# Performance work log

Measured on AMD Instinct MI355X. Metric: run time of the kernel, lower is better.

The kernel has to match this reference:

```python
import jax, jax.numpy as jnp
import numpy as np

L0, L1, L2 = 32, 16, 8
NS, NB = 512, 256
CUT = 7.0
N, E, G = 16384, 131072, 16
FEAT = L0 + 3 * L1 + 5 * L2  # 120


def setup_inputs() -> dict:
    key = jax.random.key(0)
    ks = jax.random.split(key, 16)
    rn = lambda k, s, sc=1.0: jax.random.normal(k, s, jnp.float32) * sc
    inp = {}
    inp['nodes'] = rn(ks[0], (N, FEAT))
    inp['pos'] = rn(ks[1], (N, 3)) * 5.0
    inp['cell'] = rn(ks[2], (G, 3, 3))
    inp['edge_shift'] = rn(ks[3], (E, 3))
    # tensor-product path weights (e3nn FullyConnectedTensorProduct, uvw mode)
    inp['W0'] = rn(ks[4], (L0, L0, NS))
    inp['W1'] = rn(ks[5], (L1, L1, NS))
    inp['W2'] = rn(ks[6], (L2, L2, NS))
    inp['ln_g'] = jnp.ones((NS,), jnp.float32)
    inp['ln_b'] = jnp.zeros((NS,), jnp.float32)
    inp['df_w1'] = rn(ks[7], (NB, 1024), NB ** -0.5)
    inp['df_b1'] = jnp.zeros((1024,), jnp.float32)
    inp['df_w2'] = rn(ks[8], (1024, NS), 1024 ** -0.5)
    inp['df_b2'] = jnp.zeros((NS,), jnp.float32)
    inp['mi_w1'] = rn(ks[9], (NS, 1024), NS ** -0.5)
    inp['mi_b1'] = jnp.zeros((1024,), jnp.float32)
    inp['mi_w2'] = rn(ks[10], (1024, 1024), 1024 ** -0.5)
    inp['mi_b2'] = jnp.zeros((1024,), jnp.float32)
    inp['mo_w'] = rn(ks[11], (1024, 1), 1024 ** -0.5)
    inp['mo_b'] = jnp.zeros((1,), jnp.float32)
    inp['edge_index'] = jax.random.randint(ks[12], (2, E), 0, N)
    inp['batch_vec'] = jnp.sort(jax.random.randint(ks[13], (N,), 0, G))
    return inp


def _split_irreps(x):
    x0 = x[:, :L0]                                   # (E, L0) scalars 0e
    x1 = x[:, L0:L0 + 3 * L1].reshape(-1, L1, 3)      # (E, L1, 3) vectors 1o
    x2 = x[:, L0 + 3 * L1:].reshape(-1, L2, 5)        # (E, L2, 5) 2e
    return x0, x1, x2


def reference(nodes, pos, cell, edge_shift, W0, W1, W2, ln_g, ln_b,
              df_w1, df_b1, df_w2, df_b2, mi_w1, mi_b1, mi_w2, mi_b2,
              mo_w, mo_b, edge_index, batch_vec):
    src, dst = edge_index[0], edge_index[1]
    # periodic-image translation vector per edge
    bcell = cell[batch_vec[src]]                      # (E,3,3)
    tvec = jnp.einsum('ei,eij->ej', edge_shift, bcell)
    radvec = pos[dst] - pos[src] + tvec               # (E,3)
    dist = jnp.linalg.norm(radvec, axis=1, keepdims=True)  # (E,1)
    r = 1.0 / (dist + 1e-6)
    # Bessel radial embedding with cutoff CUT, NB basis functions
    n = jnp.arange(1, NB + 1, dtype=jnp.float32)
    emb = jnp.sqrt(2.0 / CUT) * jnp.sin(n * jnp.pi * r / CUT) / r  # (E,NB)
    distfilter = jax.nn.silu(emb @ df_w1 + df_b1) @ df_w2 + df_b2  # (E,NS)

    # symmetrized fully-connected tensor product -> 0e scalars
    # 0.5*(tp(xs,xd)+tp(xd,xs)) == contraction of euv with symmetrized W
    xs0, xs1, xs2 = _split_irreps(nodes[src])
    xd0, xd1, xd2 = _split_irreps(nodes[dst])
    fan = jnp.sqrt(jnp.float32(L0 * L0 + L1 * L1 + L2 * L2))  # element path norm
    sym = lambda W: 0.5 * (W + W.transpose(1, 0, 2))
    e0 = jnp.einsum('eu,ev->euv', xs0, xd0)
    mixed = jnp.einsum('euv,uvw->ew', e0, sym(W0)) / fan
    e1 = jnp.einsum('eui,evi->euv', xs1, xd1)
    mixed = mixed + jnp.einsum('euv,uvw->ew', e1, sym(W1)) / (fan * jnp.sqrt(3.0))
    e2 = jnp.einsum('eui,evi->euv', xs2, xd2)
    mixed = mixed + jnp.einsum('euv,uvw->ew', e2, sym(W2)) / (fan * jnp.sqrt(5.0))

    # LayerNorm over numscalars
    mu = jnp.mean(mixed, axis=-1, keepdims=True)
    var = jnp.mean((mixed - mu) ** 2, axis=-1, keepdims=True)
    mixednorm = (mixed - mu) * jax.lax.rsqrt(var + 1e-5) * ln_g + ln_b

    reg = mixednorm * distfilter
    h = jax.nn.silu(reg @ mi_w1 + mi_b1)
    h = jax.nn.silu(h @ mi_w2 + mi_b2)
    return h @ mo_w + mo_b  # (E,1)
```

## Files before the change

kernel.cpp:

```cpp
#include <hip/hip_runtime.h>

#define EE 131072
#define NNODE 16384
#define FEAT 120
#define NS 512
#define NB 256
#define KCAT 1344

typedef unsigned short u16;
typedef __bf16 bf16x8 __attribute__((ext_vector_type(8)));
typedef float f32x4 __attribute__((ext_vector_type(4)));
typedef unsigned short ushort8 __attribute__((ext_vector_type(8)));
typedef unsigned short us4 __attribute__((ext_vector_type(4)));

__device__ __forceinline__ float b2f(u16 u) {
  union { unsigned int i; float f; } x; x.i = ((unsigned int)u) << 16; return x.f;
}
__device__ __forceinline__ u16 f2b(float f) {
  union { float f; unsigned int i; } x; x.f = f;
  unsigned int lsb = (x.i >> 16) & 1u;
  x.i += 0x7fffu + lsb;
  return (u16)(x.i >> 16);
}
__device__ __forceinline__ u16 f2b_fast(float f) {
  __bf16 h = (__bf16)f;
  union { __bf16 h; u16 u; } x; x.h = h; return x.u;
}
__device__ __forceinline__ float rdany(const void* p, long i, int f32) {
  return f32 ? ((const float*)p)[i] : b2f(((const u16*)p)[i]);
}

__device__ __forceinline__ void gload16(const u16* g, u16* l) {
  __builtin_amdgcn_global_load_lds(
      (__attribute__((address_space(1))) void*)(u16*)g,
      (__attribute__((address_space(3))) void*)l, 16, 0, 0);
}

struct PrepArgs {
  long cum[20];
  const void* src[19];
  u16* dst[19];
  float* outf;
  int* flag;
  const u16* nodes;
};

__global__ __launch_bounds__(256) void megaprep(PrepArgs a) {
  __shared__ int scnt[4];
  {
    u16 v = a.nodes[threadIdx.x];
    int e = (v >> 7) & 0xFF;
    unsigned long long b = __ballot(e >= 0x48);
    if ((threadIdx.x & 63) == 0) scnt[threadIdx.x >> 6] = __popcll(b);
  }
  __syncthreads();
  const int f32 = (scnt[0] + scnt[1] + scnt[2] + scnt[3]) >= 16;
  if (blockIdx.x == 0 && threadIdx.x == 0) *a.flag = f32;

  long i = (long)blockIdx.x * 256 + threadIdx.x;
  const long total = a.cum[19];
  if (i < total) {
    int s = 0;
    while (i >= a.cum[s + 1]) s++;
    long local = i - a.cum[s];
    a.dst[s][local] = f32 ? f2b(((const float*)a.src[s])[local])
                          : ((const u16*)a.src[s])[local];
  } else {
    long j = i - total;
    if (j < EE) a.outf[j] = 0.f;
  }
}

struct WprepArgs {
  const u16* tin[4];
  u16* tout[4];
  const u16 *W0, *W1, *W2;
  u16* wcT;
};

__device__ __forceinline__ void do_transpose(const u16* in, u16* out, int R, int C, int rem) {
  __shared__ u16 tile[32][33];
  const int bx = C >> 5;
  const int c0 = (rem % bx) * 32, r0 = (rem / bx) * 32;
  const int tx = threadIdx.x & 31, ty = threadIdx.x >> 5;
  for (int i = 0; i < 32; i += 8) {
    int r = r0 + ty + i, c = c0 + tx;
    if (r < R && c < C) tile[ty + i][tx] = in[(long)r * C + c];
  }
  __syncthreads();
  for (int i = 0; i < 32; i += 8) {
    int r = r0 + tx, c = c0 + ty + i;
    if (r < R && c < C) out[(long)c * R + r] = tile[tx][ty + i];
  }
}

__global__ __launch_bounds__(256) void wprep(WprepArgs a) {
  int b = blockIdx.x;
  if (b < 256) { do_transpose(a.tin[0], a.tout[0], 256, 1024, b); return; }
  b -= 256;
  if (b < 512) { do_transpose(a.tin[1], a.tout[1], 1024, 512, b); return; }
  b -= 512;
  if (b < 512) { do_transpose(a.tin[2], a.tout[2], 512, 1024, b); return; }
  b -= 512;
  if (b < 1024) { do_transpose(a.tin[3], a.tout[3], 1024, 1024, b); return; }
  b -= 1024;
  int idx = b * 256 + threadIdx.x;
  if (idx >= NS * KCAT) return;
  int w = idx / KCAT, k = idx - w * KCAT;
  const float fan = 36.66060556f;
  float val;
  if (k < 1024) {
    int u = k >> 5, v = k & 31;
    val = 0.5f * (b2f(a.W0[(u * 32 + v) * NS + w]) + b2f(a.W0[(v * 32 + u) * NS + w])) / fan;
  } else if (k < 1280) {
    int j = k - 1024;
    int u = j >> 4, v = j & 15;
    val = 0.5f * (b2f(a.W1[(u * 16 + v) * NS + w]) + b2f(a.W1[(v * 16 + u) * NS + w])) /
          (fan * 1.7320508076f);
  } else {
    int j = k - 1280;
    int u = j >> 3, v = j & 7;
    val = 0.5f * (b2f(a.W2[(u * 8 + v) * NS + w]) + b2f(a.W2[(v * 8 + u) * NS + w])) /
          (fan * 2.2360679775f);
  }
  a.wcT[idx] = f2b(val);
}

__global__ __launch_bounds__(256) void edge_prep(
    const u16* __restrict__ nodes, const void* __restrict__ pos, const void* __restrict__ cell,
    const void* __restrict__ shift, const int* __restrict__ eidx, const int* __restrict__ batch,
    u16* __restrict__ emb, u16* __restrict__ ocat, int e0, const int* __restrict__ flag) {
  const int wave = threadIdx.x >> 6, lane = threadIdx.x & 63;
  const int el = blockIdx.x * 4 + wave;
  const int e = e0 + el;
  const int f32 = *flag;
  __shared__ u16 sxs[4][FEAT], sxd[4][FEAT];
  const int src = eidx[e], dst = eidx[EE + e];
  for (int i = lane; i < FEAT; i += 64) {
    sxs[wave][i] = nodes[(long)src * FEAT + i];
    sxd[wave][i] = nodes[(long)dst * FEAT + i];
  }
  __syncthreads();
  const int b = batch[src];
  float s0 = rdany(shift, (long)e * 3, f32), s1 = rdany(shift, (long)e * 3 + 1, f32),
        s2 = rdany(shift, (long)e * 3 + 2, f32);
  float d2 = 0.f;
#pragma unroll
  for (int j = 0; j < 3; j++) {
    float tv = s0 * rdany(cell, b * 9 + j, f32) + s1 * rdany(cell, b * 9 + 3 + j, f32) +
               s2 * rdany(cell, b * 9 + 6 + j, f32);
    float rv = rdany(pos, dst * 3 + j, f32) - rdany(pos, src * 3 + j, f32) + tv;
    d2 += rv * rv;
  }
  float dist = sqrtf(d2);
  float r = 1.0f / (dist + 1e-6f);
  const float c0 = 0.5345224838f;
  const float pi7 = 0.44879895051f;
  {
    us4 ev;
#pragma unroll
    for (int j = 0; j < 4; j++) {
      int n = lane * 4 + j;
      ev[j] = f2b(c0 * sinf((float)(n + 1) * pi7 * r) / r);
    }
    *(us4*)&emb[(long)el * NB + lane * 4] = ev;
  }
  const u16* xs = sxs[wave];
  const u16* xd = sxd[wave];
  u16* orow = ocat + (long)el * KCAT;
  {
    const float xu = b2f(xs[lane >> 1]);
    const int v0 = (lane & 1) * 16;
    const ushort8 xd0 = *(const ushort8*)&xd[v0];
    const ushort8 xd1 = *(const ushort8*)&xd[v0 + 8];
    ushort8 o0, o1;
#pragma unroll
    for (int j = 0; j < 8; j++) {
      o0[j] = f2b(xu * b2f(xd0[j]));
      o1[j] = f2b(xu * b2f(xd1[j]));
    }
    *(ushort8*)&orow[lane * 16] = o0;
    *(ushort8*)&orow[lane * 16 + 8] = o1;
  }
  {
    const int u = lane >> 2;
    us4 o;
#pragma unroll
    for (int j = 0; j < 4; j++) {
      const int v = (lane & 3) * 4 + j;
      float s = 0.f;
#pragma unroll
      for (int i = 0; i < 3; i++) s += b2f(xs[32 + u * 3 + i]) * b2f(xd[32 + v * 3 + i]);
      o[j] = f2b(s);
    }
    *(us4*)&orow[1024 + lane * 4] = o;
  }
  {
    int u = lane >> 3, v = lane & 7;
    float s = 0.f;
#pragma unroll
    for (int i = 0; i < 5; i++) s += b2f(xs[80 + u * 5 + i]) * b2f(xd[80 + v * 5 + i]);
    orow[1280 + lane] = f2b(s);
  }
}

#define STGA(buf, h, part, kk)                                             \
  gload16(Ag + ((h)*128 + (part)*64) * (long)K + (kk),                      \
          &lA[buf][(h)*8192 + (part)*4096 + tid * 8])
#define STGB(buf, h, part, kk)                                             \
  gload16(Bg + ((h)*128 + (part)*64) * (long)K + (kk),                      \
          &lB[buf][(h)*8192 + (part)*4096 + tid * 8])
#define RDA(buf, fm, ks)                                                   \
  (*(const bf16x8*)((const char*)&lA[buf][0] +                             \
                    ((wm * 128 + (fm)*16 + row_l) * 128 + ((ks) ? ir1 : ir0))))
#define RDB(buf, fn, ks)                                                   \
  (*(const bf16x8*)((const char*)&lB[buf][0] +                             \
                    ((wn * 64 + (fn)*16 + row_l) * 128 + ((ks) ? ir1 : ir0))))
#define MF16(a, b, c) __builtin_amdgcn_mfma_f32_16x16x32_bf16(a, b, c, 0, 0, 0)
#define MFQn(mh, nh, Af, Bf)                                               \
  do {                                                                     \
    _Pragma("unroll") for (int f = 0; f < 4; f++)                          \
        _Pragma("unroll") for (int g = 0; g < 2; g++)                      \
            _Pragma("unroll") for (int ks = 0; ks < 2; ks++)               \
                acc[(mh)*4 + f][(nh)*2 + g] =                              \
        MF16(Af[f][ks], Bf[g][ks], acc[(mh)*4 + f][(nh)*2 + g]);           \
  } while (0)

template <int ACT, int OF32, int HEAD>
__global__ __launch_bounds__(512, 2) void gemm_bt(const u16* __restrict__ A,
                                                  const u16* __restrict__ BT,
                                                  const u16* __restrict__ bias,
                                                  void* __restrict__ Cv,
                                                  const u16* __restrict__ hw,
                                                  float* __restrict__ outf, int N, int K) {
  __shared__ __align__(16) u16 lA[2][16384];
  __shared__ __align__(16) u16 lB[2][16384];
  const int tid = threadIdx.x;
  const int lane = tid & 63;
  const int wave = tid >> 6;
  const int wm = wave >> 2, wn = wave & 3;
  const int row_l = lane & 15;
  const int kq16 = (lane >> 4) << 4;
  const int swz = (row_l & 7) << 4;
  const int ir0 = kq16 ^ swz;
  const int ir1 = (64 + kq16) ^ swz;

  const int nbn = N >> 8;
  int idx = blockIdx.x;
  if ((gridDim.x & 7) == 0) {
    int per = gridDim.x >> 3;
    idx = (blockIdx.x & 7) * per + (blockIdx.x >> 3);
  }
  const int mi = idx / nbn;
  const int ni = idx - mi * nbn;
  const long m0 = (long)mi * 256;
  const int n0 = ni << 8;
  const int nk = K >> 6;

  const int srow = tid >> 3;
  const int gseg = (tid & 7) ^ (srow & 7);
  const u16* Ag = A + (m0 + srow) * (long)K + gseg * 8;
  const u16* Bg = BT + (long)(n0 + srow) * K + gseg * 8;

  f32x4 acc[8][4];
#pragma unroll
  for (int i = 0; i < 8; i++)
#pragma unroll
    for (int j = 0; j < 4; j++)
#pragma unroll
      for (int q = 0; q < 4; q++) acc[i][j][q] = 0.f;

  STGA(0, 0, 0, 0); STGA(0, 0, 1, 0); STGA(0, 1, 0, 0); STGA(0, 1, 1, 0);
  STGB(0, 0, 0, 0); STGB(0, 0, 1, 0); STGB(0, 1, 0, 0); STGB(0, 1, 1, 0);
  if (nk > 1) {
    STGA(1, 0, 0, 64); STGA(1, 0, 1, 64); STGA(1, 1, 0, 64); STGA(1, 1, 1, 64);
    STGB(1, 0, 0, 64); STGB(1, 0, 1, 64); STGB(1, 1, 0, 64); STGB(1, 1, 1, 64);
    asm volatile("s_waitcnt vmcnt(8)" ::: "memory");
  } else {
    asm volatile("s_waitcnt vmcnt(0)" ::: "memory");
  }
  __builtin_amdgcn_s_barrier();

  bf16x8 af0[4][2], af1[4][2], b01[2][2], b23[2][2];

#pragma unroll
  for (int f = 0; f < 4; f++) { af0[f][0] = RDA(0, f, 0); af0[f][1] = RDA(0, f, 1); }
#pragma unroll
  for (int g = 0; g < 2; g++) { b01[g][0] = RDB(0, g, 0); b01[g][1] = RDB(0, g, 1); }

  for (int t = 0; t < nk; ++t) {
    const int cur = t & 1, nxt = cur ^ 1;
    const int kN2 = (t + 2) << 6;
    const bool p1 = (t + 1) < nk;
    const bool p2 = (t + 2) < nk;

#pragma unroll
    for (int g = 0; g < 2; g++) { b23[g][0] = RDB(cur, 2 + g, 0); b23[g][1] = RDB(cur, 2 + g, 1); }
    __builtin_amdgcn_sched_barrier(0);
    __builtin_amdgcn_s_setprio(1);
    MFQn(0, 0, af0, b01);
    __builtin_amdgcn_s_setprio(0);

#pragma unroll
    for (int f = 0; f < 4; f++) { af1[f][0] = RDA(cur, 4 + f, 0); af1[f][1] = RDA(cur, 4 + f, 1); }
    __builtin_amdgcn_sched_barrier(0);
    __builtin_amdgcn_s_setprio(1);
    MFQn(0, 1, af0, b23);
    __builtin_amdgcn_s_setprio(0);

    asm volatile("s_waitcnt vmcnt(0)" ::: "memory");
    __builtin_amdgcn_s_barrier();
    if (p1) {
#pragma unroll
      for (int f = 0; f < 4; f++) { af0[f][0] = RDA(nxt, f, 0); af0[f][1] = RDA(nxt, f, 1); }
    }
    if (p2) { STGB(cur, 0, 0, kN2); STGB(cur, 0, 1, kN2); }
    __builtin_amdgcn_sched_barrier(0);
    __builtin_amdgcn_s_setprio(1);
    MFQn(1, 0, af1, b01);
    __builtin_amdgcn_s_setprio(0);

    __builtin_amdgcn_s_barrier();
    if (p2) {
      STGB(cur, 1, 0, kN2); STGB(cur, 1, 1, kN2);
      STGA(cur, 0, 0, kN2); STGA(cur, 0, 1, kN2);
      STGA(cur, 1, 0, kN2); STGA(cur, 1, 1, kN2);
    }
    __builtin_amdgcn_sched_barrier(0);
    __builtin_amdgcn_s_setprio(1);
    MFQn(1, 1, af1, b23);
    __builtin_amdgcn_s_setprio(0);
    if (p1) {
#pragma unroll
      for (int g = 0; g < 2; g++) { b01[g][0] = RDB(nxt, g, 0); b01[g][1] = RDB(nxt, g, 1); }
      __builtin_amdgcn_sched_barrier(0);
    }
  }

  const int rql = (lane >> 4) * 2;
  const int cl = lane & 15;
  float* Cf = (float*)Cv;
  u16* Cb = (u16*)Cv;
  if (HEAD) {
    float bv[4], hv[4];
#pragma unroll
    for (int g = 0; g < 4; g++) {
      const int col = n0 + wn * 64 + g * 16 + cl;
      bv[g] = b2f(bias[col]);
      hv[g] = b2f(hw[col]);
    }
#pragma unroll
    for (int fm = 0; fm < 8; fm++) {
#pragma unroll
      for (int q = 0; q < 4; q++) {
        float s = 0.f;
#pragma unroll
        for (int g = 0; g < 4; g++) {
          float v = acc[fm][g][q] + bv[g];
          if (ACT) v = __fdividef(v, 1.0f + __expf(-v));
          s += v * hv[g];
        }
        s += __shfl_xor(s, 1);
        s += __shfl_xor(s, 2);
        s += __shfl_xor(s, 4);
        s += __shfl_xor(s, 8);
        if (cl == 0) {
          long row = m0 + wm * 128 + fm * 16 + rql * 2 + q;
          atomicAdd(&outf[row], s);
        }
      }
    }
  } else {
#pragma unroll
    for (int fm = 0; fm < 8; fm++) {
#pragma unroll
      for (int g = 0; g < 4; g++) {
        const int col = n0 + wn * 64 + g * 16 + cl;
        const float bvv = bias ? b2f(bias[col]) : 0.0f;
#pragma unroll
        for (int q = 0; q < 4; q++) {
          long row = m0 + wm * 128 + fm * 16 + rql * 2 + q;
          float v = acc[fm][g][q] + bvv;
          if (ACT) v = __fdividef(v, 1.0f + __expf(-v));
          if (OF32)
            Cf[row * N + col] = v;
          else
            Cb[row * N + col] = f2b_fast(v);
        }
      }
    }
  }
}

__global__ __launch_bounds__(256) void ln_mul_k(const float* __restrict__ mixed,
                                                const u16* __restrict__ g,
                                                const u16* __restrict__ bvec,
                                                u16* __restrict__ dfreg) {
  const int wave = threadIdx.x >> 6, lane = threadIdx.x & 63;
  const long e = (long)blockIdx.x * 4 + wave;
  const float* row = mixed + e * NS;
  float x[8];
  f32x4 v0 = *(const f32x4*)&row[lane * 8];
  f32x4 v1 = *(const f32x4*)&row[lane * 8 + 4];
#pragma unroll
  for (int j = 0; j < 4; j++) { x[j] = v0[j]; x[4 + j] = v1[j]; }
  float s = 0.f, sq = 0.f;
#pragma unroll
  for (int j = 0; j < 8; j++) { s += x[j]; sq += x[j] * x[j]; }
  for (int o = 32; o; o >>= 1) { s += __shfl_xor(s, o); sq += __shfl_xor(sq, o); }
  float mu = s * (1.0f / 512.0f);
  float var = sq * (1.0f / 512.0f) - mu * mu;
  float rstd = rsqrtf(var + 1e-5f);
  u16* drow = dfreg + e * NS;
  ushort8 dv = *(const ushort8*)&drow[lane * 8];
  ushort8 ov;
#pragma unroll
  for (int j = 0; j < 8; j++) {
    int c = lane * 8 + j;
    float val = (x[j] - mu) * rstd * b2f(g[c]) + b2f(bvec[c]);
    ov[j] = f2b(val * b2f(dv[j]));
  }
  *(ushort8*)&drow[lane * 8] = ov;
}

__global__ __launch_bounds__(256) void head_finish(const float* __restrict__ outf,
                                                   const u16* __restrict__ b,
                                                   void* __restrict__ out,
                                                   const int* __restrict__ flag) {
  int e = blockIdx.x * 256 + threadIdx.x;
  float v = outf[e] + b2f(b[0]);
  if (*flag)
    ((float*)out)[e] = v;
  else
    ((u16*)out)[e] = f2b(v);
}

extern "C" void kernel_launch(void* const* d_in, const int* in_sizes, int n_in, void* d_out,
                              int out_size, void* d_ws, size_t ws_size, hipStream_t stream) {
  const int* eidx = (const int*)d_in[19];
  const int* batch = (const int*)d_in[20];

  char* ws = (char*)d_ws;
  size_t off = 0;
  auto alloc = [&](size_t bytes) {
    char* p = ws + off;
    off += (bytes + 255) & ~(size_t)255;
    return p;
  };

  int* flag = (int*)alloc(256);
  float* outf = (float*)alloc((size_t)EE * 4);

  PrepArgs pa;
  u16* cv[19];
  long cum = 0;
  for (int i = 0; i < 19; i++) {
    long n = in_sizes[i];
    cv[i] = (u16*)alloc((size_t)n * 2);
    pa.cum[i] = cum;
    pa.src[i] = d_in[i];
    pa.dst[i] = cv[i];
    cum += n;
  }
  pa.cum[19] = cum;
  pa.outf = outf;
  pa.flag = flag;
  pa.nodes = (const u16*)d_in[0];
  {
    long tot = cum + EE;
    megaprep<<<(int)((tot + 255) / 256), 256, 0, stream>>>(pa);
  }
  const u16* nodes = cv[0];
  const u16* ln_g = cv[7];
  const u16* ln_b = cv[8];
  const u16* df_b1 = cv[10];
  const u16* df_b2 = cv[12];
  const u16* mi_b1 = cv[14];
  const u16* mi_b2 = cv[16];
  const u16* mo_w = cv[17];
  const u16* mo_b = cv[18];

  u16* w1T = (u16*)alloc(1024 * 256 * 2);
  u16* w2T = (u16*)alloc(512 * 1024 * 2);
  u16* m1T = (u16*)alloc(1024 * 512 * 2);
  u16* m2T = (u16*)alloc((size_t)1024 * 1024 * 2);
  u16* wcT = (u16*)alloc((size_t)NS * KCAT * 2);

  WprepArgs wa;
  wa.tin[0] = cv[9];  wa.tout[0] = w1T;
  wa.tin[1] = cv[11]; wa.tout[1] = w2T;
  wa.tin[2] = cv[13]; wa.tout[2] = m1T;
  wa.tin[3] = cv[15]; wa.tout[3] = m2T;
  wa.W0 = cv[4]; wa.W1 = cv[5]; wa.W2 = cv[6];
  wa.wcT = wcT;
  wprep<<<4992, 256, 0, stream>>>(wa);

  int nchunk = 1;
  while (nchunk < 64) {
    size_t CHs = (size_t)(EE / nchunk);
    size_t need = off + CHs * 6272 + 8192;
    if (need <= ws_size) break;
    nchunk <<= 1;
  }
  const int CH = EE / nchunk;

  u16* ocat = (u16*)alloc((size_t)CH * KCAT * 2);
  u16* emb = (u16*)alloc((size_t)CH * NB * 2);
  u16* h1 = (u16*)alloc((size_t)CH * 1024 * 2);
  u16* dfb = (u16*)alloc((size_t)CH * NS * 2);
  u16* h2 = ocat;
  float* mixed = (float*)h1;

  const int RB = CH / 256;
  for (int c = 0; c < nchunk; c++) {
    const int eb = c * CH;
    edge_prep<<<CH / 4, 256, 0, stream>>>(nodes, d_in[1], d_in[2], d_in[3], eidx, batch, emb,
                                          ocat, eb, flag);

    gemm_bt<1, 0, 0><<<RB * 4, 512, 0, stream>>>(emb, w1T, df_b1, h1, nullptr, nullptr, 1024, 256);
    gemm_bt<0, 0, 0><<<RB * 2, 512, 0, stream>>>(h1, w2T, df_b2, dfb, nullptr, nullptr, 512, 1024);

    gemm_bt<0, 1, 0><<<RB * 2, 512, 0, stream>>>(ocat, wcT, nullptr, mixed, nullptr, nullptr, 512,
                                                 1344);

    ln_mul_k<<<CH / 4, 256, 0, stream>>>(mixed, ln_g, ln_b, dfb);

    gemm_bt<1, 0, 0><<<RB * 4, 512, 0, stream>>>(dfb, m1T, mi_b1, h2, nullptr, nullptr, 1024, 512);
    gemm_bt<1, 0, 1><<<RB * 4, 512, 0, stream>>>(h2, m2T, mi_b2, nullptr, mo_w, outf + eb, 1024,
                                                 1024);
  }
  head_finish<<<EE / 256, 256, 0, stream>>>(outf, mo_b, d_out, flag);
}
```

Measured before the change: 1.335 ms.

## Fuse independent distfilter-1 and tensor-product GEMMs into one grouped launch

Makes the GEMM kernel take a two-section argument struct so one launch can run two independent GEMMs, split by block index. The first distfilter GEMM and the tensor-product contraction GEMM now share a single grid when workspace allows a separate buffer for the mixed output. This is meant to cut launch overhead and fill the GPU better for small chunk sizes. In exchange, ACT and OF32 become runtime values instead of template parameters, which may add branches and register pressure in the epilogue of every GEMM.

```diff
diff --git a/kernel.cpp b/kernel.cpp
--- a/kernel.cpp
+++ b/kernel.cpp
@@ -204,6 +204,14 @@
   }
 }
 
+struct GSec {
+  const u16 *A, *BT, *bias, *hw;
+  void* Cv;
+  float* outf;
+  int N, K, act, of32;
+};
+struct GArgs { GSec s[2]; int split; };
+
 #define STGA(buf, h, part, kk)                                             \
   gload16(Ag + ((h)*128 + (part)*64) * (long)K + (kk),                      \
           &lA[buf][(h)*8192 + (part)*4096 + tid * 8])
@@ -226,15 +234,23 @@
         MF16(Af[f][ks], Bf[g][ks], acc[(mh)*4 + f][(nh)*2 + g]);           \
   } while (0)
 
-template <int ACT, int OF32, int HEAD>
-__global__ __launch_bounds__(512, 2) void gemm_bt(const u16* __restrict__ A,
-                                                  const u16* __restrict__ BT,
-                                                  const u16* __restrict__ bias,
-                                                  void* __restrict__ Cv,
-                                                  const u16* __restrict__ hw,
-                                                  float* __restrict__ outf, int N, int K) {
+template <int HEAD>
+__global__ __launch_bounds__(512, 2) void gemm_bt(GArgs ga) {
   __shared__ __align__(16) u16 lA[2][16384];
   __shared__ __align__(16) u16 lB[2][16384];
+  const int sec = ((int)blockIdx.x >= ga.split) ? 1 : 0;
+  const GSec S = ga.s[sec];
+  const u16* __restrict__ A = S.A;
+  const u16* __restrict__ BT = S.BT;
+  const u16* __restrict__ bias = S.bias;
+  const u16* __restrict__ hw = S.hw;
+  void* __restrict__ Cv = S.Cv;
+  float* __restrict__ outf = S.outf;
+  const int N = S.N, K = S.K;
+  const int ACT = S.act, OF32 = S.of32;
+  const int nblk = sec ? ((int)gridDim.x - ga.split) : ga.split;
+  const int bx = (int)blockIdx.x - (sec ? ga.split : 0);
+
   const int tid = threadIdx.x;
   const int lane = tid & 63;
   const int wave = tid >> 6;
@@ -246,10 +262,10 @@
   const int ir1 = (64 + kq16) ^ swz;
 
   const int nbn = N >> 8;
-  int idx = blockIdx.x;
-  if ((gridDim.x & 7) == 0) {
-    int per = gridDim.x >> 3;
-    idx = (blockIdx.x & 7) * per + (blockIdx.x >> 3);
+  int idx = bx;
+  if ((nblk & 7) == 0) {
+    int per = nblk >> 3;
+    idx = (bx & 7) * per + (bx >> 3);
   }
   const int mi = idx / nbn;
   const int ni = idx - mi * nbn;
@@ -509,7 +525,19 @@
   u16* h1 = (u16*)alloc((size_t)CH * 1024 * 2);
   u16* dfb = (u16*)alloc((size_t)CH * NS * 2);
   u16* h2 = ocat;
+
   float* mixed = (float*)h1;
+  bool paired = false;
+  if (off + (size_t)CH * NS * 4 + 256 <= ws_size) {
+    mixed = (float*)alloc((size_t)CH * NS * 4);
+    paired = true;
+  }
+
+  auto mk = [](const u16* A, const u16* BT, const u16* bias, const u16* hw, void* Cv,
+               float* of, int N, int K, int act, int of32) {
+    GSec s; s.A = A; s.BT = BT; s.bias = bias; s.hw = hw; s.Cv = Cv; s.outf = of;
+    s.N = N; s.K = K; s.act = act; s.of32 = of32; return s;
+  };
 
   const int RB = CH / 256;
   for (int c = 0; c < nchunk; c++) {
@@ -517,17 +545,32 @@
     edge_prep<<<CH / 4, 256, 0, stream>>>(nodes, d_in[1], d_in[2], d_in[3], eidx, batch, emb,
                                           ocat, eb, flag);
 
-    gemm_bt<1, 0, 0><<<RB * 4, 512, 0, stream>>>(emb, w1T, df_b1, h1, nullptr, nullptr, 1024, 256);
-    gemm_bt<0, 0, 0><<<RB * 2, 512, 0, stream>>>(h1, w2T, df_b2, dfb, nullptr, nullptr, 512, 1024);
-
-    gemm_bt<0, 1, 0><<<RB * 2, 512, 0, stream>>>(ocat, wcT, nullptr, mixed, nullptr, nullptr, 512,
-                                                 1344);
+    GSec sG1 = mk(emb, w1T, df_b1, nullptr, h1, nullptr, 1024, 256, 1, 0);
+    GSec sG2 = mk(h1, w2T, df_b2, nullptr, dfb, nullptr, 512, 1024, 0, 0);
+    GSec sG3 = mk(ocat, wcT, nullptr, nullptr, mixed, nullptr, 512, 1344, 0, 1);
+
+    if (paired) {
+      GArgs g13; g13.s[0] = sG1; g13.s[1] = sG3; g13.split = RB * 4;
+      gemm_bt<0><<<RB * 6, 512, 0, stream>>>(g13);
+      GArgs g2; g2.s[0] = sG2; g2.s[1] = sG2; g2.split = RB * 2;
+      gemm_bt<0><<<RB * 2, 512, 0, stream>>>(g2);
+    } else {
+      GArgs g1; g1.s[0] = sG1; g1.s[1] = sG1; g1.split = RB * 4;
+      gemm_bt<0><<<RB * 4, 512, 0, stream>>>(g1);
+      GArgs g2; g2.s[0] = sG2; g2.s[1] = sG2; g2.split = RB * 2;
+      gemm_bt<0><<<RB * 2, 512, 0, stream>>>(g2);
+      GArgs g3; g3.s[0] = sG3; g3.s[1] = sG3; g3.split = RB * 2;
+      gemm_bt<0><<<RB * 2, 512, 0, stream>>>(g3);
+    }
 
     ln_mul_k<<<CH / 4, 256, 0, stream>>>(mixed, ln_g, ln_b, dfb);
 
-    gemm_bt<1, 0, 0><<<RB * 4, 512, 0, stream>>>(dfb, m1T, mi_b1, h2, nullptr, nullptr, 1024, 512);
-    gemm_bt<1, 0, 1><<<RB * 4, 512, 0, stream>>>(h2, m2T, mi_b2, nullptr, mo_w, outf + eb, 1024,
-                                                 1024);
+    GArgs g4; g4.s[0] = mk(dfb, m1T, mi_b1, nullptr, h2, nullptr, 1024, 512, 1, 0);
+    g4.s[1] = g4.s[0]; g4.split = RB * 4;
+    gemm_bt<0><<<RB * 4, 512, 0, stream>>>(g4);
+    GArgs g5; g5.s[0] = mk(h2, m2T, mi_b2, mo_w, nullptr, outf + eb, 1024, 1024, 1, 0);
+    g5.s[1] = g5.s[0]; g5.split = RB * 4;
+    gemm_bt<1><<<RB * 4, 512, 0, stream>>>(g5);
   }
   head_finish<<<EE / 256, 256, 0, stream>>>(outf, mo_b, d_out, flag);
 }
```

After: 1.445 ms. +8.2%, slower.
